# Kernel optimization log

Measured on AMD Instinct MI355X. Metric: run time of the kernel, lower is better.

Reference implementation:

```python
import jax, jax.numpy as jnp
import numpy as np

DIM = 1024
HEADS = 8


def setup_inputs() -> dict:
    key = jax.random.key(0)
    ks = jax.random.split(key, 8)
    b, n, m, nc, d = 2, 1024, 4, 1024, DIM
    x = jax.random.normal(ks[0], (b, n, d), dtype=jnp.float32)
    context = jax.random.normal(ks[1], (b, m, nc, d), dtype=jnp.float32)
    doc_similarities = jax.random.normal(ks[2], (b, m), dtype=jnp.float32)
    # learned params (Linear weights stored as [in, out] for x @ W)
    s = 1.0 / np.sqrt(d)
    Wq = jax.random.uniform(ks[3], (d, d), minval=-s, maxval=s, dtype=jnp.float32)
    Wkv = jax.random.uniform(ks[4], (d, 2 * d), minval=-s, maxval=s, dtype=jnp.float32)
    Wout = jax.random.uniform(ks[5], (d, d), minval=-s, maxval=s, dtype=jnp.float32)
    bout = jax.random.uniform(ks[6], (d,), minval=-s, maxval=s, dtype=jnp.float32)
    beta = jnp.array(1.0, dtype=jnp.float32)
    return {"x": x, "context": context, "doc_similarities": doc_similarities,
            "Wq": Wq, "Wkv": Wkv, "beta": beta, "Wout": Wout, "bout": bout}


def reference(x, context, doc_similarities, Wq, Wkv, beta, Wout, bout):
    b, n, dim = x.shape
    h = HEADS
    hd = dim // h
    scale = dim ** -0.5
    m, nc = context.shape[1], context.shape[2]

    # q: [b, h, n, hd]
    q = (x @ Wq).reshape(b, n, h, hd).transpose(0, 2, 1, 3)

    # flatten docs: [b, m*nc, dim]
    ctx = context.reshape(b, m * nc, dim)
    # doc similarity bias, repeated per token within each doc: [b, m*nc]
    sim = jnp.repeat(doc_similarities, nc, axis=1) * beta

    kv = ctx @ Wkv  # [b, L, 2*dim]
    k, v = jnp.split(kv, 2, axis=-1)
    k = k.reshape(b, m * nc, h, hd).transpose(0, 2, 1, 3)  # [b, h, L, hd]
    v = v.reshape(b, m * nc, h, hd).transpose(0, 2, 1, 3)

    dots = jnp.einsum('bhid,bhjd->bhij', q, k) * scale
    dots = dots + sim[:, None, None, :]
    attn = jax.nn.softmax(dots, axis=-1)
    out = jnp.einsum('bhij,bhjd->bhid', attn, v)
    out = out.transpose(0, 2, 1, 3).reshape(b, n, dim)
    return out @ Wout + bout
```

## Files before the change

kernel.cpp:

```cpp
#include <hip/hip_runtime.h>
#include <stdint.h>

typedef __attribute__((ext_vector_type(4))) float f32x4;
typedef __attribute__((ext_vector_type(8))) __bf16 bf16x8;

__device__ __forceinline__ uint16_t f2bf(float f) {
  uint32_t u = __builtin_bit_cast(uint32_t, f);
  u += 0x7FFFu + ((u >> 16) & 1u);
  return (uint16_t)(u >> 16);
}

__device__ __forceinline__ float bf2f(uint16_t u) {
  uint32_t v = ((uint32_t)u) << 16;
  return __builtin_bit_cast(float, v);
}

__device__ __forceinline__ void load_lds16(const uint16_t* g, uint16_t* l) {
  __builtin_amdgcn_global_load_lds((const __attribute__((address_space(1))) void*)g,
                                   (__attribute__((address_space(3))) void*)l, 16, 0, 0);
}

__global__ __launch_bounds__(256) void k_convert2(const float* __restrict__ x,
                                                  const float* __restrict__ ctx,
                                                  uint16_t* __restrict__ xb,
                                                  uint16_t* __restrict__ ctxb) {
  int i = blockIdx.x * 256 + threadIdx.x;
  const float* in;
  uint16_t* out;
  int j;
  if (i < 524288) { in = x; out = xb; j = i; }
  else            { in = ctx; out = ctxb; j = i - 524288; }
  float4 v = ((const float4*)in)[j];
  union { uint16_t u[4]; uint64_t q; } o;
  o.u[0] = f2bf(v.x); o.u[1] = f2bf(v.y); o.u[2] = f2bf(v.z); o.u[3] = f2bf(v.w);
  ((uint64_t*)out)[j] = o.q;
}

__global__ __launch_bounds__(256) void k_prep_w(const float* __restrict__ Wq,
                                                const float* __restrict__ Wkv,
                                                const float* __restrict__ Wout,
                                                uint16_t* __restrict__ wqt,
                                                uint16_t* __restrict__ wkvt,
                                                uint16_t* __restrict__ woutt,
                                                float qscale) {
  __shared__ float tile[32][33];
  const int K = 1024;
  int bx = blockIdx.x;
  const float* W;
  uint16_t* Wt;
  int N;
  float sc;
  if (blockIdx.z == 0) {
    if (bx < 32) { W = Wq; Wt = wqt; N = 1024; sc = qscale; }
    else         { W = Wout; Wt = woutt; N = 1024; sc = 1.0f; bx -= 32; }
  } else         { W = Wkv; Wt = wkvt; N = 2048; sc = 1.0f; }
  int n0 = bx * 32, k0 = blockIdx.y * 32;
  int c = threadIdx.x & 31, r0 = threadIdx.x >> 5;
#pragma unroll
  for (int i = 0; i < 4; i++) {
    int r = r0 + i * 8;
    tile[r][c] = W[(size_t)(k0 + r) * N + n0 + c];
  }
  __syncthreads();
#pragma unroll
  for (int i = 0; i < 4; i++) {
    int r = r0 + i * 8;
    Wt[(size_t)(n0 + r) * K + k0 + c] = f2bf(tile[c][r] * sc);
  }
}

__global__ __launch_bounds__(256) void k_gemm_kv(const uint16_t* __restrict__ A,
                                                 const uint16_t* __restrict__ Bt,
                                                 uint16_t* __restrict__ kb,
                                                 uint16_t* __restrict__ vtb) {
  __shared__ uint16_t smem[9216];
  uint16_t* la = smem;
  uint16_t* lb = smem + 4096;
  const int K = 1024;
  const int tid = threadIdx.x;
  const int lane = tid & 63, w = tid >> 6;
  const int quad = lane >> 4, l16 = lane & 15;
  const int wr = (w >> 1) * 64, wc = (w & 1) * 64;
  const int bx = blockIdx.x, by = blockIdx.y;
  const size_t tr0 = (size_t)by * 128, tc0 = (size_t)bx * 128;
  f32x4 acc[4][4] = {};
  const int rA = tid >> 2, slotA = tid & 3;
  const int rA1 = rA + 64;
  const int segA0 = (slotA ^ ((rA + (rA >> 2)) & 3)) * 8;
  const int segA1 = (slotA ^ ((rA1 + (rA1 >> 2)) & 3)) * 8;
  const uint16_t* Ab = A + tr0 * K;
  const uint16_t* Bb = Bt + tc0 * K;
  for (int k0 = 0; k0 < K; k0 += 32) {
    __syncthreads();
    load_lds16(Ab + (size_t)rA * K + k0 + segA0, la + tid * 8);
    load_lds16(Ab + (size_t)rA1 * K + k0 + segA1, la + (tid + 256) * 8);
    load_lds16(Bb + (size_t)rA * K + k0 + segA0, lb + tid * 8);
    load_lds16(Bb + (size_t)rA1 * K + k0 + segA1, lb + (tid + 256) * 8);
    __syncthreads();
    bf16x8 af[4], bfr[4];
#pragma unroll
    for (int i = 0; i < 4; i++) {
      int R = wr + i * 16 + l16;
      int s = quad ^ ((R + (R >> 2)) & 3);
      af[i] = *(const bf16x8*)&la[R * 32 + s * 8];
    }
#pragma unroll
    for (int j = 0; j < 4; j++) {
      int R = wc + j * 16 + l16;
      int s = quad ^ ((R + (R >> 2)) & 3);
      bfr[j] = *(const bf16x8*)&lb[R * 32 + s * 8];
    }
#pragma unroll
    for (int i = 0; i < 4; i++)
#pragma unroll
      for (int j = 0; j < 4; j++)
        acc[i][j] = __builtin_amdgcn_mfma_f32_16x16x32_bf16(af[i], bfr[j], acc[i][j], 0, 0, 0);
  }
  __syncthreads();
  if (bx < 8) {
#pragma unroll
    for (int i = 0; i < 4; i++)
#pragma unroll
      for (int j = 0; j < 4; j++) {
        size_t row = tr0 + wr + i * 16 + quad * 4;
        size_t col = tc0 + wc + j * 16 + l16;
#pragma unroll
        for (int r = 0; r < 4; r++)
          kb[(row + r) * 1024 + col] = f2bf(acc[i][j][r]);
      }
  } else {
    const int bh = (by >> 5) * 8 + (bx - 8);
    const int lbase = (by & 31) * 128;
    uint16_t* vdst = vtb + (size_t)bh * 524288;
#pragma unroll
    for (int half = 0; half < 2; half++) {
      if (wr == half * 64) {
#pragma unroll
        for (int i = 0; i < 4; i++)
#pragma unroll
          for (int j = 0; j < 4; j++) {
            int rowl = i * 16 + quad * 4;
            int col = wc + j * 16 + l16;
            union { uint64_t q; uint16_t u[4]; } pk;
#pragma unroll
            for (int r = 0; r < 4; r++) pk.u[r] = f2bf(acc[i][j][r]);
            *(uint64_t*)&smem[col * 72 + rowl] = pk.q;
          }
      }
      __syncthreads();
      {
        int col = tid >> 1, rseg = (tid & 1) * 32;
        const uint16_t* src = &smem[col * 72 + rseg];
        uint16_t* d = vdst + (size_t)col * 4096 + lbase + half * 64 + rseg;
#pragma unroll
        for (int k = 0; k < 4; k++)
          ((uint4*)d)[k] = *(const uint4*)&src[k * 8];
      }
      __syncthreads();
    }
  }
}

template <int F32OUT>
__global__ __launch_bounds__(256) void k_gemm64(const uint16_t* __restrict__ A,
                                                const uint16_t* __restrict__ Bt,
                                                uint16_t* __restrict__ Cb,
                                                float* __restrict__ Cf,
                                                const float* __restrict__ bias,
                                                int M, int N, int K) {
  __shared__ uint16_t la[64 * 64];
  __shared__ uint16_t lb[64 * 64];
  const int tid = threadIdx.x;
  const int lane = tid & 63, w = tid >> 6;
  const int quad = lane >> 4, l16 = lane & 15;
  const int wr = (w >> 1) * 32, wc = (w & 1) * 32;
  const size_t tr0 = (size_t)blockIdx.y * 64, tc0 = (size_t)blockIdx.x * 64;
  f32x4 acc[2][2] = {};
  const int rS = tid >> 3, sS = tid & 7;
  const int seg = (sS ^ (rS & 7)) * 8;
  const uint16_t* Ab = A + tr0 * K;
  const uint16_t* Bb = Bt + tc0 * K;
  for (int k0 = 0; k0 < K; k0 += 64) {
    __syncthreads();
    load_lds16(Ab + (size_t)rS * K + k0 + seg, la + tid * 8);
    load_lds16(Ab + (size_t)(rS + 32) * K + k0 + seg, la + (tid + 256) * 8);
    load_lds16(Bb + (size_t)rS * K + k0 + seg, lb + tid * 8);
    load_lds16(Bb + (size_t)(rS + 32) * K + k0 + seg, lb + (tid + 256) * 8);
    __syncthreads();
#pragma unroll
    for (int sub = 0; sub < 2; sub++) {
      const int kk = sub * 4 + quad;
      bf16x8 af[2], bfr[2];
#pragma unroll
      for (int i = 0; i < 2; i++) {
        int R = wr + i * 16 + l16;
        af[i] = *(const bf16x8*)&la[R * 64 + (kk ^ (R & 7)) * 8];
      }
#pragma unroll
      for (int j = 0; j < 2; j++) {
        int R = wc + j * 16 + l16;
        bfr[j] = *(const bf16x8*)&lb[R * 64 + (kk ^ (R & 7)) * 8];
      }
#pragma unroll
      for (int i = 0; i < 2; i++)
#pragma unroll
        for (int j = 0; j < 2; j++)
          acc[i][j] = __builtin_amdgcn_mfma_f32_16x16x32_bf16(af[i], bfr[j], acc[i][j], 0, 0, 0);
    }
  }
#pragma unroll
  for (int i = 0; i < 2; i++) {
#pragma unroll
    for (int j = 0; j < 2; j++) {
      size_t row = tr0 + wr + i * 16 + quad * 4;
      size_t col = tc0 + wc + j * 16 + l16;
#pragma unroll
      for (int r = 0; r < 4; r++) {
        if constexpr (F32OUT)
          Cf[(row + r) * N + col] = acc[i][j][r] + bias[col];
        else
          Cb[(row + r) * N + col] = f2bf(acc[i][j][r]);
      }
    }
  }
}

__global__ __launch_bounds__(256) void k_attn(const uint16_t* __restrict__ q,
                                              const uint16_t* __restrict__ kb,
                                              const uint16_t* __restrict__ vt,
                                              const float* __restrict__ sims,
                                              const float* __restrict__ beta,
                                              uint16_t* __restrict__ po,
                                              float* __restrict__ pm,
                                              float* __restrict__ pl) {
  __shared__ uint16_t Kl[64 * 128];
  __shared__ uint16_t Vl[128 * 64];
  __shared__ uint16_t Pl[4 * 32 * 64];
  __shared__ uint16_t Ol[16 * 64];
  const int bz = blockIdx.z, b = bz >> 2, sp = bz & 3;
  const int h = blockIdx.y, q0 = blockIdx.x * 128;
  const int tid = threadIdx.x, lane = tid & 63, w = tid >> 6;
  const int quad = lane >> 4, l16 = lane & 15;
  const float simv_l2 = sims[b * 4 + sp] * beta[0] * 1.44269504f;
  uint16_t* Pw = Pl + w * 2048;

  *(uint64_t*)&Ol[tid * 4] = 0x3F803F803F803F80ull;

  bf16x8 qf[2][4];
#pragma unroll
  for (int rb = 0; rb < 2; rb++) {
    const uint16_t* qrow =
        q + ((size_t)(b * 1024 + q0 + w * 32 + rb * 16 + l16)) * 1024 + h * 128 + quad * 8;
#pragma unroll
    for (int ks = 0; ks < 4; ks++) qf[rb][ks] = *(const bf16x8*)(qrow + ks * 32);
  }
  f32x4 o[2][8] = {};
  f32x4 o9[2] = {};

  const uint16_t* kptr = kb + ((size_t)(b * 4096 + sp * 1024)) * 1024 + h * 128;
  const uint16_t* vptr = vt + ((size_t)(b * 8 + h) * 128) * 4096 + sp * 1024;

  for (int c = 0; c < 16; c++) {
    __syncthreads();
#pragma unroll
    for (int ii = 0; ii < 4; ii++) {
      int g = tid + ii * 256;
      int row = g >> 4, seg = (g & 15) ^ (row & 15);
      load_lds16(kptr + (size_t)row * 1024 + seg * 8, Kl + g * 8);
    }
#pragma unroll
    for (int ii = 0; ii < 4; ii++) {
      int g = tid + ii * 256;
      int row = g >> 3, seg = (g & 7) ^ (row & 7);
      load_lds16(vptr + (size_t)row * 4096 + seg * 8, Vl + g * 8);
    }
    __syncthreads();
#pragma unroll
    for (int nb = 0; nb < 4; nb++) {
      f32x4 s0 = {}, s1 = {};
#pragma unroll
      for (int ks = 0; ks < 4; ks++) {
        bf16x8 kf = *(const bf16x8*)&Kl[(nb * 16 + l16) * 128 + (((ks * 4 + quad) ^ l16) * 8)];
        s0 = __builtin_amdgcn_mfma_f32_16x16x32_bf16(qf[0][ks], kf, s0, 0, 0, 0);
        s1 = __builtin_amdgcn_mfma_f32_16x16x32_bf16(qf[1][ks], kf, s1, 0, 0, 0);
      }
      const int s_lin = nb * 2 + (l16 >> 3);
#pragma unroll
      for (int r = 0; r < 4; r++) {
        int rp0 = quad * 4 + r;
        Pw[rp0 * 64 + ((s_lin ^ (rp0 & 7)) * 8) + (l16 & 7)] =
            f2bf(__builtin_amdgcn_exp2f(s0[r]));
        int rp1 = 16 + rp0;
        Pw[rp1 * 64 + ((s_lin ^ (rp1 & 7)) * 8) + (l16 & 7)] =
            f2bf(__builtin_amdgcn_exp2f(s1[r]));
      }
    }
    __asm__ volatile("s_waitcnt lgkmcnt(0)" ::: "memory");
#pragma unroll
    for (int ks = 0; ks < 2; ks++) {
      const int sq = ((ks * 4 + quad) ^ (l16 & 7)) * 8;
      bf16x8 pf0 = *(const bf16x8*)&Pw[l16 * 64 + sq];
      bf16x8 pf1 = *(const bf16x8*)&Pw[(16 + l16) * 64 + sq];
#pragma unroll
      for (int nb = 0; nb < 8; nb++) {
        bf16x8 vf = *(const bf16x8*)&Vl[(nb * 16 + l16) * 64 + sq];
        o[0][nb] = __builtin_amdgcn_mfma_f32_16x16x32_bf16(pf0, vf, o[0][nb], 0, 0, 0);
        o[1][nb] = __builtin_amdgcn_mfma_f32_16x16x32_bf16(pf1, vf, o[1][nb], 0, 0, 0);
      }
      bf16x8 of = *(const bf16x8*)&Ol[l16 * 64 + sq];
      o9[0] = __builtin_amdgcn_mfma_f32_16x16x32_bf16(pf0, of, o9[0], 0, 0, 0);
      o9[1] = __builtin_amdgcn_mfma_f32_16x16x32_bf16(pf1, of, o9[1], 0, 0, 0);
    }
    kptr += (size_t)64 * 1024;
    vptr += 64;
  }
  const int rowbase = (sp * 16 + b * 8 + h) * 1024 + q0 + w * 32;
#pragma unroll
  for (int rb = 0; rb < 2; rb++)
#pragma unroll
    for (int r = 0; r < 4; r++) {
      int row = rowbase + rb * 16 + quad * 4 + r;
#pragma unroll
      for (int nb = 0; nb < 8; nb++)
        po[(size_t)row * 128 + nb * 16 + l16] = f2bf(o[rb][nb][r]);
      if (l16 == 0) {
        pm[row] = simv_l2;
        pl[row] = o9[rb][r];
      }
    }
}

__global__ __launch_bounds__(256) void k_merge(const uint16_t* __restrict__ po,
                                               const float* __restrict__ pm,
                                               const float* __restrict__ pl,
                                               uint16_t* __restrict__ attb) {
  const int bq = blockIdx.x;
  const int b = bq >> 10, qi = bq & 1023;
  const int t = threadIdx.x;
  const int h = t >> 5, d0 = (t & 31) * 4;
  const int bh = b * 8 + h;
  float m[4];
  float M = -INFINITY;
#pragma unroll
  for (int s = 0; s < 4; s++) {
    m[s] = pm[(s * 16 + bh) * 1024 + qi];
    M = fmaxf(M, m[s]);
  }
  float den = 0.f, wgt[4];
#pragma unroll
  for (int s = 0; s < 4; s++) {
    wgt[s] = __builtin_amdgcn_exp2f(m[s] - M);
    den += wgt[s] * pl[(s * 16 + bh) * 1024 + qi];
  }
  const float inv = 1.0f / den;
  float acc[4] = {0.f, 0.f, 0.f, 0.f};
#pragma unroll
  for (int s = 0; s < 4; s++) {
    const uint16_t* p = &po[(((size_t)(s * 16 + bh)) * 1024 + qi) * 128 + d0];
    union { uint64_t q; uint16_t u[4]; } v;
    v.q = *(const uint64_t*)p;
#pragma unroll
    for (int j = 0; j < 4; j++) acc[j] += wgt[s] * bf2f(v.u[j]);
  }
  union { uint64_t q; uint16_t u[4]; } o;
#pragma unroll
  for (int j = 0; j < 4; j++) o.u[j] = f2bf(acc[j] * inv);
  *(uint64_t*)&attb[((size_t)(b * 1024 + qi)) * 1024 + h * 128 + d0] = o.q;
}

extern "C" void kernel_launch(void* const* d_in, const int* in_sizes, int n_in,
                              void* d_out, int out_size, void* d_ws, size_t ws_size,
                              hipStream_t stream) {
  (void)in_sizes; (void)n_in; (void)out_size; (void)ws_size;
  const float* x    = (const float*)d_in[0];
  const float* ctx  = (const float*)d_in[1];
  const float* sims = (const float*)d_in[2];
  const float* Wq   = (const float*)d_in[3];
  const float* Wkv  = (const float*)d_in[4];
  const float* beta = (const float*)d_in[5];
  const float* Wout = (const float*)d_in[6];
  const float* bout = (const float*)d_in[7];
  float* out = (float*)d_out;

  char* ws = (char*)d_ws;
  uint16_t* xb    = (uint16_t*)(ws + 0);
  uint16_t* ctxb  = (uint16_t*)(ws + (4u << 20));
  uint16_t* wqt   = (uint16_t*)(ws + (20u << 20));
  uint16_t* wkvt  = (uint16_t*)(ws + (22u << 20));
  uint16_t* woutt = (uint16_t*)(ws + (26u << 20));
  uint16_t* qb    = (uint16_t*)(ws + (28u << 20));
  uint16_t* kb    = (uint16_t*)(ws + (32u << 20));
  uint16_t* vtb   = (uint16_t*)(ws + (48u << 20));
  uint16_t* attb  = (uint16_t*)(ws + (64u << 20));
  uint16_t* po = (uint16_t*)(ws + 0);
  float*    pm = (float*)(ws + (16u << 20));
  float*    pl = (float*)(ws + (16u << 20) + (256u << 10));

  const float LOG2E = 1.44269504f;
  const float qscale = 0.03125f * LOG2E;

  k_convert2<<<10240, 256, 0, stream>>>(x, ctx, xb, ctxb);
  k_prep_w<<<dim3(64, 32, 2), 256, 0, stream>>>(Wq, Wkv, Wout, wqt, wkvt, woutt, qscale);
  k_gemm64<0><<<dim3(16, 32), 256, 0, stream>>>(xb, wqt, qb, nullptr, nullptr, 2048, 1024, 1024);
  k_gemm_kv<<<dim3(16, 64), 256, 0, stream>>>(ctxb, wkvt, kb, vtb);
  k_attn<<<dim3(8, 8, 8), 256, 0, stream>>>(qb, kb, vtb, sims, beta, po, pm, pl);
  k_merge<<<2048, 256, 0, stream>>>(po, pm, pl, attb);
  k_gemm64<1><<<dim3(16, 32), 256, 0, stream>>>(attb, woutt, nullptr, out, bout, 2048, 1024, 1024);
}
```

Before: 241.5 us.

## Fuse prep kernels and Q/KV GEMMs, double-buffer K/V tiles in attention

Merges the input conversion and weight transpose kernels into one launch, and folds the Q projection GEMM into the KV GEMM launch with 128x128 tiles. That removes two kernel launches and lets the Q tiles share the machine with the KV tiles. The attention kernel now double-buffers its K/V LDS tiles so the next chunk loads while the current one computes. It also replaces the LDS ones-matrix used for the row-sum MFMA with a register constant. LDS use in attention roughly doubles, which may reduce occupancy.

```diff
diff --git a/kernel.cpp b/kernel.cpp
--- a/kernel.cpp
+++ b/kernel.cpp
@@ -20,42 +20,44 @@
                                    (__attribute__((address_space(3))) void*)l, 16, 0, 0);
 }
 
-__global__ __launch_bounds__(256) void k_convert2(const float* __restrict__ x,
-                                                  const float* __restrict__ ctx,
-                                                  uint16_t* __restrict__ xb,
-                                                  uint16_t* __restrict__ ctxb) {
-  int i = blockIdx.x * 256 + threadIdx.x;
-  const float* in;
-  uint16_t* out;
-  int j;
-  if (i < 524288) { in = x; out = xb; j = i; }
-  else            { in = ctx; out = ctxb; j = i - 524288; }
-  float4 v = ((const float4*)in)[j];
-  union { uint16_t u[4]; uint64_t q; } o;
-  o.u[0] = f2bf(v.x); o.u[1] = f2bf(v.y); o.u[2] = f2bf(v.z); o.u[3] = f2bf(v.w);
-  ((uint64_t*)out)[j] = o.q;
-}
-
-__global__ __launch_bounds__(256) void k_prep_w(const float* __restrict__ Wq,
-                                                const float* __restrict__ Wkv,
-                                                const float* __restrict__ Wout,
-                                                uint16_t* __restrict__ wqt,
-                                                uint16_t* __restrict__ wkvt,
-                                                uint16_t* __restrict__ woutt,
-                                                float qscale) {
+__global__ __launch_bounds__(256) void k_prep(const float* __restrict__ x,
+                                              const float* __restrict__ ctx,
+                                              const float* __restrict__ Wq,
+                                              const float* __restrict__ Wkv,
+                                              const float* __restrict__ Wout,
+                                              uint16_t* __restrict__ xb,
+                                              uint16_t* __restrict__ ctxb,
+                                              uint16_t* __restrict__ wqt,
+                                              uint16_t* __restrict__ wkvt,
+                                              uint16_t* __restrict__ woutt,
+                                              float qscale) {
   __shared__ float tile[32][33];
-  const int K = 1024;
-  int bx = blockIdx.x;
+  int id = blockIdx.x;
+  int tid = threadIdx.x;
+  if (id < 10240) {
+    const float* in;
+    uint16_t* out;
+    int j = id * 256 + tid;
+    if (j < 524288) { in = x; out = xb; }
+    else            { in = ctx; out = ctxb; j -= 524288; }
+    float4 v = ((const float4*)in)[j];
+    union { uint16_t u[4]; uint64_t q; } o;
+    o.u[0] = f2bf(v.x); o.u[1] = f2bf(v.y); o.u[2] = f2bf(v.z); o.u[3] = f2bf(v.w);
+    ((uint64_t*)out)[j] = o.q;
+    return;
+  }
+  id -= 10240;
   const float* W;
   uint16_t* Wt;
-  int N;
-  float sc;
-  if (blockIdx.z == 0) {
-    if (bx < 32) { W = Wq; Wt = wqt; N = 1024; sc = qscale; }
-    else         { W = Wout; Wt = woutt; N = 1024; sc = 1.0f; bx -= 32; }
-  } else         { W = Wkv; Wt = wkvt; N = 2048; sc = 1.0f; }
-  int n0 = bx * 32, k0 = blockIdx.y * 32;
-  int c = threadIdx.x & 31, r0 = threadIdx.x >> 5;
+  int N, n0, k0;
+  float sc = 1.0f;
+  if (id < 1024)      { W = Wq;   Wt = wqt;   N = 1024; sc = qscale;
+                        n0 = (id & 31) * 32; k0 = (id >> 5) * 32; }
+  else if (id < 2048) { W = Wout; Wt = woutt; N = 1024; id -= 1024;
+                        n0 = (id & 31) * 32; k0 = (id >> 5) * 32; }
+  else                { W = Wkv;  Wt = wkvt;  N = 2048; id -= 2048;
+                        n0 = (id & 63) * 32; k0 = (id >> 6) * 32; }
+  int c = tid & 31, r0 = tid >> 5;
 #pragma unroll
   for (int i = 0; i < 4; i++) {
     int r = r0 + i * 8;
@@ -65,14 +67,17 @@
 #pragma unroll
   for (int i = 0; i < 4; i++) {
     int r = r0 + i * 8;
-    Wt[(size_t)(n0 + r) * K + k0 + c] = f2bf(tile[c][r] * sc);
-  }
-}
-
-__global__ __launch_bounds__(256) void k_gemm_kv(const uint16_t* __restrict__ A,
-                                                 const uint16_t* __restrict__ Bt,
-                                                 uint16_t* __restrict__ kb,
-                                                 uint16_t* __restrict__ vtb) {
+    Wt[(size_t)(n0 + r) * 1024 + k0 + c] = f2bf(tile[c][r] * sc);
+  }
+}
+
+__global__ __launch_bounds__(256) void k_gemm_fused(const uint16_t* __restrict__ ctxb,
+                                                    const uint16_t* __restrict__ wkvt,
+                                                    const uint16_t* __restrict__ xb,
+                                                    const uint16_t* __restrict__ wqt,
+                                                    uint16_t* __restrict__ kb,
+                                                    uint16_t* __restrict__ vtb,
+                                                    uint16_t* __restrict__ qb) {
   __shared__ uint16_t smem[9216];
   uint16_t* la = smem;
   uint16_t* lb = smem + 4096;
@@ -81,15 +86,23 @@
   const int lane = tid & 63, w = tid >> 6;
   const int quad = lane >> 4, l16 = lane & 15;
   const int wr = (w >> 1) * 64, wc = (w & 1) * 64;
-  const int bx = blockIdx.x, by = blockIdx.y;
-  const size_t tr0 = (size_t)by * 128, tc0 = (size_t)bx * 128;
+  int id = blockIdx.x;
+  int bx, by, isQ;
+  const uint16_t *Ab, *Bb;
+  if (id < 1024) {
+    isQ = 0; bx = id & 15; by = id >> 4;
+    Ab = ctxb + (size_t)by * 128 * K;
+    Bb = wkvt + (size_t)bx * 128 * K;
+  } else {
+    isQ = 1; id -= 1024; bx = id & 7; by = id >> 3;
+    Ab = xb + (size_t)by * 128 * K;
+    Bb = wqt + (size_t)bx * 128 * K;
+  }
   f32x4 acc[4][4] = {};
   const int rA = tid >> 2, slotA = tid & 3;
   const int rA1 = rA + 64;
   const int segA0 = (slotA ^ ((rA + (rA >> 2)) & 3)) * 8;
   const int segA1 = (slotA ^ ((rA1 + (rA1 >> 2)) & 3)) * 8;
-  const uint16_t* Ab = A + tr0 * K;
-  const uint16_t* Bb = Bt + tc0 * K;
   for (int k0 = 0; k0 < K; k0 += 32) {
     __syncthreads();
     load_lds16(Ab + (size_t)rA * K + k0 + segA0, la + tid * 8);
@@ -117,13 +130,24 @@
         acc[i][j] = __builtin_amdgcn_mfma_f32_16x16x32_bf16(af[i], bfr[j], acc[i][j], 0, 0, 0);
   }
   __syncthreads();
-  if (bx < 8) {
+  if (isQ) {
 #pragma unroll
     for (int i = 0; i < 4; i++)
 #pragma unroll
       for (int j = 0; j < 4; j++) {
-        size_t row = tr0 + wr + i * 16 + quad * 4;
-        size_t col = tc0 + wc + j * 16 + l16;
+        size_t row = (size_t)by * 128 + wr + i * 16 + quad * 4;
+        size_t col = (size_t)bx * 128 + wc + j * 16 + l16;
+#pragma unroll
+        for (int r = 0; r < 4; r++)
+          qb[(row + r) * 1024 + col] = f2bf(acc[i][j][r]);
+      }
+  } else if (bx < 8) {
+#pragma unroll
+    for (int i = 0; i < 4; i++)
+#pragma unroll
+      for (int j = 0; j < 4; j++) {
+        size_t row = (size_t)by * 128 + wr + i * 16 + quad * 4;
+        size_t col = (size_t)bx * 128 + wc + j * 16 + l16;
 #pragma unroll
         for (int r = 0; r < 4; r++)
           kb[(row + r) * 1024 + col] = f2bf(acc[i][j][r]);
@@ -161,10 +185,8 @@
   }
 }
 
-template <int F32OUT>
 __global__ __launch_bounds__(256) void k_gemm64(const uint16_t* __restrict__ A,
                                                 const uint16_t* __restrict__ Bt,
-                                                uint16_t* __restrict__ Cb,
                                                 float* __restrict__ Cf,
                                                 const float* __restrict__ bias,
                                                 int M, int N, int K) {
@@ -215,12 +237,8 @@
       size_t row = tr0 + wr + i * 16 + quad * 4;
       size_t col = tc0 + wc + j * 16 + l16;
 #pragma unroll
-      for (int r = 0; r < 4; r++) {
-        if constexpr (F32OUT)
-          Cf[(row + r) * N + col] = acc[i][j][r] + bias[col];
-        else
-          Cb[(row + r) * N + col] = f2bf(acc[i][j][r]);
-      }
+      for (int r = 0; r < 4; r++)
+        Cf[(row + r) * N + col] = acc[i][j][r] + bias[col];
     }
   }
 }
@@ -233,10 +251,9 @@
                                               uint16_t* __restrict__ po,
                                               float* __restrict__ pm,
                                               float* __restrict__ pl) {
-  __shared__ uint16_t Kl[64 * 128];
-  __shared__ uint16_t Vl[128 * 64];
-  __shared__ uint16_t Pl[4 * 32 * 64];
-  __shared__ uint16_t Ol[16 * 64];
+  __shared__ uint16_t Kl[2][8192];
+  __shared__ uint16_t Vl[2][8192];
+  __shared__ uint16_t Pl[4 * 2048];
   const int bz = blockIdx.z, b = bz >> 2, sp = bz & 3;
   const int h = blockIdx.y, q0 = blockIdx.x * 128;
   const int tid = threadIdx.x, lane = tid & 63, w = tid >> 6;
@@ -244,7 +261,10 @@
   const float simv_l2 = sims[b * 4 + sp] * beta[0] * 1.44269504f;
   uint16_t* Pw = Pl + w * 2048;
 
-  *(uint64_t*)&Ol[tid * 4] = 0x3F803F803F803F80ull;
+  union { uint32_t u[4]; bf16x8 v; } Oc;
+#pragma unroll
+  for (int j = 0; j < 4; j++) Oc.u[j] = 0x3F803F80u;
+  const bf16x8 onesf = Oc.v;
 
   bf16x8 qf[2][4];
 #pragma unroll
@@ -257,30 +277,40 @@
   f32x4 o[2][8] = {};
   f32x4 o9[2] = {};
 
-  const uint16_t* kptr = kb + ((size_t)(b * 4096 + sp * 1024)) * 1024 + h * 128;
-  const uint16_t* vptr = vt + ((size_t)(b * 8 + h) * 128) * 4096 + sp * 1024;
-
-  for (int c = 0; c < 16; c++) {
-    __syncthreads();
+  const uint16_t* kbase = kb + ((size_t)(b * 4096 + sp * 1024)) * 1024 + h * 128;
+  const uint16_t* vbase = vt + ((size_t)(b * 8 + h) * 128) * 4096 + sp * 1024;
+
+  auto stage = [&](int c, int bi) {
+    const uint16_t* kc = kbase + (size_t)c * 64 * 1024;
+    const uint16_t* vc = vbase + c * 64;
+    uint16_t* Kb = Kl[bi];
+    uint16_t* Vb = Vl[bi];
 #pragma unroll
     for (int ii = 0; ii < 4; ii++) {
       int g = tid + ii * 256;
       int row = g >> 4, seg = (g & 15) ^ (row & 15);
-      load_lds16(kptr + (size_t)row * 1024 + seg * 8, Kl + g * 8);
+      load_lds16(kc + (size_t)row * 1024 + seg * 8, Kb + g * 8);
     }
 #pragma unroll
     for (int ii = 0; ii < 4; ii++) {
       int g = tid + ii * 256;
       int row = g >> 3, seg = (g & 7) ^ (row & 7);
-      load_lds16(vptr + (size_t)row * 4096 + seg * 8, Vl + g * 8);
-    }
+      load_lds16(vc + (size_t)row * 4096 + seg * 8, Vb + g * 8);
+    }
+  };
+
+  stage(0, 0);
+  for (int c = 0; c < 16; c++) {
     __syncthreads();
+    if (c < 15) stage(c + 1, (c + 1) & 1);
+    const uint16_t* Kb = Kl[c & 1];
+    const uint16_t* Vb = Vl[c & 1];
 #pragma unroll
     for (int nb = 0; nb < 4; nb++) {
       f32x4 s0 = {}, s1 = {};
 #pragma unroll
       for (int ks = 0; ks < 4; ks++) {
-        bf16x8 kf = *(const bf16x8*)&Kl[(nb * 16 + l16) * 128 + (((ks * 4 + quad) ^ l16) * 8)];
+        bf16x8 kf = *(const bf16x8*)&Kb[(nb * 16 + l16) * 128 + (((ks * 4 + quad) ^ l16) * 8)];
         s0 = __builtin_amdgcn_mfma_f32_16x16x32_bf16(qf[0][ks], kf, s0, 0, 0, 0);
         s1 = __builtin_amdgcn_mfma_f32_16x16x32_bf16(qf[1][ks], kf, s1, 0, 0, 0);
       }
@@ -303,16 +333,13 @@
       bf16x8 pf1 = *(const bf16x8*)&Pw[(16 + l16) * 64 + sq];
 #pragma unroll
       for (int nb = 0; nb < 8; nb++) {
-        bf16x8 vf = *(const bf16x8*)&Vl[(nb * 16 + l16) * 64 + sq];
+        bf16x8 vf = *(const bf16x8*)&Vb[(nb * 16 + l16) * 64 + sq];
         o[0][nb] = __builtin_amdgcn_mfma_f32_16x16x32_bf16(pf0, vf, o[0][nb], 0, 0, 0);
         o[1][nb] = __builtin_amdgcn_mfma_f32_16x16x32_bf16(pf1, vf, o[1][nb], 0, 0, 0);
       }
-      bf16x8 of = *(const bf16x8*)&Ol[l16 * 64 + sq];
-      o9[0] = __builtin_amdgcn_mfma_f32_16x16x32_bf16(pf0, of, o9[0], 0, 0, 0);
-      o9[1] = __builtin_amdgcn_mfma_f32_16x16x32_bf16(pf1, of, o9[1], 0, 0, 0);
-    }
-    kptr += (size_t)64 * 1024;
-    vptr += 64;
+      o9[0] = __builtin_amdgcn_mfma_f32_16x16x32_bf16(pf0, onesf, o9[0], 0, 0, 0);
+      o9[1] = __builtin_amdgcn_mfma_f32_16x16x32_bf16(pf1, onesf, o9[1], 0, 0, 0);
+    }
   }
   const int rowbase = (sp * 16 + b * 8 + h) * 1024 + q0 + w * 32;
 #pragma unroll
@@ -399,11 +426,9 @@
   const float LOG2E = 1.44269504f;
   const float qscale = 0.03125f * LOG2E;
 
-  k_convert2<<<10240, 256, 0, stream>>>(x, ctx, xb, ctxb);
-  k_prep_w<<<dim3(64, 32, 2), 256, 0, stream>>>(Wq, Wkv, Wout, wqt, wkvt, woutt, qscale);
-  k_gemm64<0><<<dim3(16, 32), 256, 0, stream>>>(xb, wqt, qb, nullptr, nullptr, 2048, 1024, 1024);
-  k_gemm_kv<<<dim3(16, 64), 256, 0, stream>>>(ctxb, wkvt, kb, vtb);
+  k_prep<<<14336, 256, 0, stream>>>(x, ctx, Wq, Wkv, Wout, xb, ctxb, wqt, wkvt, woutt, qscale);
+  k_gemm_fused<<<1152, 256, 0, stream>>>(ctxb, wkvt, xb, wqt, kb, vtb, qb);
   k_attn<<<dim3(8, 8, 8), 256, 0, stream>>>(qb, kb, vtb, sims, beta, po, pm, pl);
   k_merge<<<2048, 256, 0, stream>>>(po, pm, pl, attb);
-  k_gemm64<1><<<dim3(16, 32), 256, 0, stream>>>(attb, woutt, nullptr, out, bout, 2048, 1024, 1024);
-}
+  k_gemm64<<<dim3(16, 32), 256, 0, stream>>>(attb, woutt, out, bout, 2048, 1024, 1024);
+}
```

After: 232.8 us. 1.04x faster.
